# Performance work log

Hardware: AMD Instinct MI355X
Metric: run time of the kernel (lower is better)

The kernel has to match this reference:

```python
import jax, jax.numpy as jnp
import numpy as np

NEG = -1e30  # finite stand-in for -inf in the sparse-softmax mask


def setup_inputs() -> dict:
    key = jax.random.key(0)
    kh, kwl, kwn, kn = jax.random.split(key, 4)
    B, S, D, E = 8, 4096, 1024, 64
    return {
        "h": jax.random.normal(kh, (B, S, D), dtype=jnp.float32),
        "Wl": jax.random.normal(kwl, (E, D), dtype=jnp.float32) * 0.02,
        "bl": jnp.zeros((E,), dtype=jnp.float32),
        "Wn": jax.random.normal(kwn, (E, D), dtype=jnp.float32) * 0.02,
        "bn": jnp.zeros((E,), dtype=jnp.float32),
        "noise": jax.random.normal(kn, (B, S, E), dtype=jnp.float32),
        "top_k": 2,
    }


def reference(h, Wl, bl, Wn, bn, noise, top_k):
    # logits, noise std: two small linears over the expert dim
    logits = jnp.einsum("bsd,ed->bse", h, Wl) + bl          # [B,S,E]
    std = jax.nn.softplus(jnp.einsum("bsd,ed->bse", h, Wn) + bn)
    noisy = logits + noise * std                              # [B,S,E]

    full_p = jax.nn.softmax(noisy, axis=-1)

    topk_vals, ix = jax.lax.top_k(noisy, top_k)               # [B,S,k]
    E = noisy.shape[-1]
    # scatter top-k values back into a -inf-filled tensor == mask non-topk
    mask = jax.nn.one_hot(ix, E, dtype=jnp.bool_).any(axis=-2)  # [B,S,E]
    sparse = jnp.where(mask, noisy, NEG)
    route_p = jax.nn.softmax(sparse, axis=-1)
    return route_p, ix, full_p
```

## Files before the change

### kernel.cpp

```cpp
#include <hip/hip_runtime.h>
#include <math.h>


#define DIM 1024
#define NEXP 64
#define CS 132
#define LOSCALE 2048.0f
#define INV_LOSCALE (1.0f / 2048.0f)

using half8v   = __attribute__((ext_vector_type(8)))  _Float16;
using floatx16 = __attribute__((ext_vector_type(16))) float;

#define MFMA32(a, b, c) __builtin_amdgcn_mfma_f32_32x32x16_f16((a), (b), (c), 0, 0, 0)

__global__ __launch_bounds__(512)
void prep_B(const float* __restrict__ Wl, const float* __restrict__ Wn,
            _Float16* __restrict__ Bp)
{
    const int idx = blockIdx.x * 512 + threadIdx.x;
    const int r  = idx >> 7;
    const int c2 = idx & 127;
    const float* W = (r < 64) ? (Wl + (size_t)r * DIM) : (Wn + (size_t)(r - 64) * DIM);
    float f[8];
    *(float4*)(f)     = *(const float4*)(W + c2 * 8);
    *(float4*)(f + 4) = *(const float4*)(W + c2 * 8 + 4);
    half8v hi, lo;
#pragma unroll
    for (int i = 0; i < 8; i++) {
        _Float16 hh = (_Float16)f[i];
        hi[i] = hh;
        lo[i] = (_Float16)((f[i] - (float)hh) * LOSCALE);
    }
    const int t = c2 >> 1, hf = c2 & 1;
    _Float16* base = Bp + ((size_t)t * 128 + r) * 32 + hf * 16;
    *(half8v*)(base)     = hi;
    *(half8v*)(base + 8) = lo;
}

__global__ __launch_bounds__(256, 4)
void router_fused(const float* __restrict__ h, const _Float16* __restrict__ Bp,
                  const float* __restrict__ bl, const float* __restrict__ bn,
                  const float* __restrict__ noise,
                  float* __restrict__ outR, float* __restrict__ outIx,
                  float* __restrict__ outF)
{
    __shared__ float Cs[32 * CS];

    const int tid   = threadIdx.x;
    const int wv    = tid >> 6;
    const int lane  = tid & 63;
    const int row31 = lane & 31;
    const int oct   = lane >> 5;
    const int colb  = wv * 32;
    const int tok0  = blockIdx.x * 32;

    const float*    aP = h  + (size_t)(tok0 + row31) * DIM + oct * 8;
    const _Float16* bP = Bp + (size_t)(colb + row31) * 32 + oct * 16;

    floatx16 acc1, acc2;
#pragma unroll
    for (int i = 0; i < 16; i++) { acc1[i] = 0.f; acc2[i] = 0.f; }

#define LOADA(s, A0, A1) do {                                                  \
        (A0) = *(const float4*)(aP + (s) * 16);                                \
        (A1) = *(const float4*)(aP + (s) * 16 + 4);                            \
    } while (0)
#define LOADB(s, BH, BL) do {                                                  \
        (BH) = *(const half8v*)(bP + (size_t)(s) * 4096);                      \
        (BL) = *(const half8v*)(bP + (size_t)(s) * 4096 + 8);                  \
    } while (0)
#define STEP(A0, A1, BH, BL) do {                                              \
        float f_[8] = {(A0).x, (A0).y, (A0).z, (A0).w,                         \
                       (A1).x, (A1).y, (A1).z, (A1).w};                        \
        half8v aH_, aL_;                                                       \
        _Pragma("unroll")                                                      \
        for (int i_ = 0; i_ < 8; i_++) {                                       \
            _Float16 hh_ = (_Float16)f_[i_];                                   \
            aH_[i_] = hh_;                                                     \
            aL_[i_] = (_Float16)((f_[i_] - (float)hh_) * LOSCALE);             \
        }                                                                      \
        acc1 = MFMA32(aH_, (BH), acc1);                                        \
        acc2 = MFMA32(aH_, (BL), acc2);                                        \
        acc2 = MFMA32(aL_, (BH), acc2);                                        \
    } while (0)

    float4 aE0, aE1, aO0, aO1;
    half8v bHE, bLE, bHO, bLO;
    LOADA(0, aE0, aE1); LOADB(0, bHE, bLE);
    LOADA(1, aO0, aO1); LOADB(1, bHO, bLO);

    for (int tb = 0; tb < 31; ++tb) {
        const int s = 2 * tb;
        STEP(aE0, aE1, bHE, bLE);
        LOADA(s + 2, aE0, aE1); LOADB(s + 2, bHE, bLE);
        STEP(aO0, aO1, bHO, bLO);
        LOADA(s + 3, aO0, aO1); LOADB(s + 3, bHO, bLO);
    }
    STEP(aE0, aE1, bHE, bLE);
    STEP(aO0, aO1, bHO, bLO);

#undef STEP
#undef LOADB
#undef LOADA

#pragma unroll
    for (int i = 0; i < 16; i++) {
        const int rowt = (i & 3) + 8 * (i >> 2) + 4 * oct;
        Cs[rowt * CS + colb + row31] = acc1[i] + acc2[i] * INV_LOSCALE;
    }
    __syncthreads();

    const float blv = bl[lane];
    const float bnv = bn[lane];

    for (int t = wv; t < 32; t += 4) {
        const int gt = tok0 + t;
        float xr = Cs[t * CS + lane] + blv;
        float xf = Cs[t * CS + 64 + lane] + bnv;
        float nz = noise[(size_t)gt * NEXP + lane];

        float stdv = fmaxf(xf, 0.f) + log1pf(expf(-fabsf(xf)));
        float noisy = fmaf(nz, stdv, xr);

        float v = noisy; int idx = lane;
#pragma unroll
        for (int o = 32; o > 0; o >>= 1) {
            float ov = __shfl_xor(v, o, 64);
            int   oi = __shfl_xor(idx, o, 64);
            if (ov > v || (ov == v && oi < idx)) { v = ov; idx = oi; }
        }
        const float v1 = v; const int i1 = idx;

        float p = expf(noisy - v1);
        float s = p;
#pragma unroll
        for (int o = 32; o > 0; o >>= 1) s += __shfl_xor(s, o, 64);
        float fullp = p / s;

        v = (lane == i1) ? -INFINITY : noisy; idx = lane;
#pragma unroll
        for (int o = 32; o > 0; o >>= 1) {
            float ov = __shfl_xor(v, o, 64);
            int   oi = __shfl_xor(idx, o, 64);
            if (ov > v || (ov == v && oi < idx)) { v = ov; idx = oi; }
        }
        const float v2 = v; const int i2 = idx;

        float e2 = expf(v2 - v1);
        float den = 1.f + e2;
        float routep = (lane == i1) ? (1.f / den) : ((lane == i2) ? (e2 / den) : 0.f);

        outR[(size_t)gt * NEXP + lane] = routep;
        outF[(size_t)gt * NEXP + lane] = fullp;
        if (lane == 0) {
            outIx[(size_t)gt * 2 + 0] = (float)i1;
            outIx[(size_t)gt * 2 + 1] = (float)i2;
        }
    }
}

extern "C" void kernel_launch(void* const* d_in, const int* in_sizes, int n_in,
                              void* d_out, int out_size, void* d_ws, size_t ws_size,
                              hipStream_t stream) {
    const float* h     = (const float*)d_in[0];
    const float* Wl    = (const float*)d_in[1];
    const float* bl    = (const float*)d_in[2];
    const float* Wn    = (const float*)d_in[3];
    const float* bn    = (const float*)d_in[4];
    const float* noise = (const float*)d_in[5];
    float* out = (float*)d_out;

    const int M = in_sizes[0] / DIM;
    float* outR  = out;
    float* outIx = out + (size_t)M * NEXP;
    float* outF  = outIx + (size_t)M * 2;

    _Float16* Bp = (_Float16*)d_ws;

    prep_B<<<32, 512, 0, stream>>>(Wl, Wn, Bp);
    router_fused<<<M / 32, 256, 0, stream>>>(h, Bp, bl, bn, noise, outR, outIx, outF);
}
```

Measured before the change: 293.3 us.

## Stage A tile hi/lo split once into double-buffered LDS shared across waves

Previously every wave loaded the same 32 token rows of h from global memory and redid the fp32-to-fp16 hi/lo split, giving 4x redundant loads and conversions per block. Now the block loads A cooperatively, splits it once, writes it to double-buffered LDS, and each wave reads its MFMA operands from LDS while the next tile is loaded and converted. This adds a barrier per 64-wide K tile and LDS traffic. The LDS is reused as the output staging buffer afterwards.

```diff
diff --git a/kernel.cpp b/kernel.cpp
--- a/kernel.cpp
+++ b/kernel.cpp
@@ -7,11 +7,17 @@
 #define CS 132
 #define LOSCALE 2048.0f
 #define INV_LOSCALE (1.0f / 2048.0f)
+#define AROW 272
+#define ABUF 8704
 
 using half8v   = __attribute__((ext_vector_type(8)))  _Float16;
 using floatx16 = __attribute__((ext_vector_type(16))) float;
 
 #define MFMA32(a, b, c) __builtin_amdgcn_mfma_f32_32x32x16_f16((a), (b), (c), 0, 0, 0)
+
+#define WAITLGKM0 asm volatile("s_waitcnt lgkmcnt(0)" ::: "memory")
+#define SCHED0    __builtin_amdgcn_sched_barrier(0)
+#define BAR       __builtin_amdgcn_s_barrier()
 
 __global__ __launch_bounds__(512)
 void prep_B(const float* __restrict__ Wl, const float* __restrict__ Wn,
@@ -44,7 +50,7 @@
                   float* __restrict__ outR, float* __restrict__ outIx,
                   float* __restrict__ outF)
 {
-    __shared__ float Cs[32 * CS];
+    __shared__ __align__(16) char lds_raw[2 * ABUF];
 
     const int tid   = threadIdx.x;
     const int wv    = tid >> 6;
@@ -54,55 +60,107 @@
     const int colb  = wv * 32;
     const int tok0  = blockIdx.x * 32;
 
-    const float*    aP = h  + (size_t)(tok0 + row31) * DIM + oct * 8;
+    const int rSt = tid >> 3, f8 = tid & 7;
+    const float* aStage = h + (size_t)(tok0 + rSt) * DIM + f8 * 8;
+    const int aWhi = rSt * AROW + f8 * 16;
+
     const _Float16* bP = Bp + (size_t)(colb + row31) * 32 + oct * 16;
 
+    const int rdHi = row31 * AROW;
+
     floatx16 acc1, acc2;
 #pragma unroll
     for (int i = 0; i < 16; i++) { acc1[i] = 0.f; acc2[i] = 0.f; }
 
-#define LOADA(s, A0, A1) do {                                                  \
-        (A0) = *(const float4*)(aP + (s) * 16);                                \
-        (A1) = *(const float4*)(aP + (s) * 16 + 4);                            \
-    } while (0)
-#define LOADB(s, BH, BL) do {                                                  \
-        (BH) = *(const half8v*)(bP + (size_t)(s) * 4096);                      \
-        (BL) = *(const half8v*)(bP + (size_t)(s) * 4096 + 8);                  \
-    } while (0)
-#define STEP(A0, A1, BH, BL) do {                                              \
+#define LOADA(t, A0, A1) do {                                                  \
+        (A0) = *(const float4*)(aStage + (t) * 64);                            \
+        (A1) = *(const float4*)(aStage + (t) * 64 + 4);                        \
+    } while (0)
+
+#define SPLITW(bufc, A0, A1) do {                                              \
         float f_[8] = {(A0).x, (A0).y, (A0).z, (A0).w,                         \
                        (A1).x, (A1).y, (A1).z, (A1).w};                        \
-        half8v aH_, aL_;                                                       \
+        half8v hi_, lo_;                                                       \
         _Pragma("unroll")                                                      \
         for (int i_ = 0; i_ < 8; i_++) {                                       \
             _Float16 hh_ = (_Float16)f_[i_];                                   \
-            aH_[i_] = hh_;                                                     \
-            aL_[i_] = (_Float16)((f_[i_] - (float)hh_) * LOSCALE);             \
+            hi_[i_] = hh_;                                                     \
+            lo_[i_] = (_Float16)((f_[i_] - (float)hh_) * LOSCALE);             \
         }                                                                      \
+        *(half8v*)((bufc) + aWhi)       = hi_;                                 \
+        *(half8v*)((bufc) + aWhi + 128) = lo_;                                 \
+    } while (0)
+
+#define ISSUE_B(t) do {                                                        \
+        const _Float16* bs_ = bP + (size_t)(t) * 16384;                        \
+        bh0 = *(const half8v*)(bs_);                                           \
+        bl0 = *(const half8v*)(bs_ + 8);                                       \
+        bh1 = *(const half8v*)(bs_ + 4096);                                    \
+        bl1 = *(const half8v*)(bs_ + 4104);                                    \
+        bh2 = *(const half8v*)(bs_ + 8192);                                    \
+        bl2 = *(const half8v*)(bs_ + 8200);                                    \
+        bh3 = *(const half8v*)(bs_ + 12288);                                   \
+        bl3 = *(const half8v*)(bs_ + 12296);                                   \
+    } while (0)
+
+#define SUBSTEP(bufc, ss, BH, BL) do {                                         \
+        const int co_ = ((ss) * 2 + oct) << 4;                                 \
+        const half8v aH_ = *(const half8v*)((bufc) + rdHi + co_);              \
+        const half8v aL_ = *(const half8v*)((bufc) + rdHi + co_ + 128);        \
         acc1 = MFMA32(aH_, (BH), acc1);                                        \
         acc2 = MFMA32(aH_, (BL), acc2);                                        \
         acc2 = MFMA32(aL_, (BH), acc2);                                        \
     } while (0)
 
+#define COMPUTE(bufc) do {                                                     \
+        SUBSTEP(bufc, 0, bh0, bl0);                                            \
+        SUBSTEP(bufc, 1, bh1, bl1);                                            \
+        SUBSTEP(bufc, 2, bh2, bl2);                                            \
+        SUBSTEP(bufc, 3, bh3, bl3);                                            \
+    } while (0)
+
+    half8v bh0, bl0, bh1, bl1, bh2, bl2, bh3, bl3;
+    char* const buf0 = lds_raw;
+    char* const buf1 = lds_raw + ABUF;
     float4 aE0, aE1, aO0, aO1;
-    half8v bHE, bLE, bHO, bLO;
-    LOADA(0, aE0, aE1); LOADB(0, bHE, bLE);
-    LOADA(1, aO0, aO1); LOADB(1, bHO, bLO);
-
-    for (int tb = 0; tb < 31; ++tb) {
-        const int s = 2 * tb;
-        STEP(aE0, aE1, bHE, bLE);
-        LOADA(s + 2, aE0, aE1); LOADB(s + 2, bHE, bLE);
-        STEP(aO0, aO1, bHO, bLO);
-        LOADA(s + 3, aO0, aO1); LOADB(s + 3, bHO, bLO);
-    }
-    STEP(aE0, aE1, bHE, bLE);
-    STEP(aO0, aO1, bHO, bLO);
-
-#undef STEP
-#undef LOADB
+
+    LOADA(0, aE0, aE1);
+    SPLITW(buf0, aE0, aE1);
+    LOADA(1, aO0, aO1);
+    WAITLGKM0; SCHED0;
+    BAR; SCHED0;
+
+#define BODY_W_L(t, CBUF, NBUF, AW0, AW1, AL0, AL1) do {                       \
+        ISSUE_B(t);                                                            \
+        SPLITW(NBUF, AW0, AW1);                                                \
+        LOADA((t) + 2, AL0, AL1);                                              \
+        COMPUTE(CBUF);                                                         \
+        WAITLGKM0; SCHED0;                                                     \
+        BAR; SCHED0;                                                           \
+    } while (0)
+
+    for (int tb = 0; tb < 7; ++tb) {
+        const int t0 = 2 * tb;
+        BODY_W_L(t0,     buf0, buf1, aO0, aO1, aE0, aE1);
+        BODY_W_L(t0 + 1, buf1, buf0, aE0, aE1, aO0, aO1);
+    }
+    ISSUE_B(14);
+    SPLITW(buf1, aO0, aO1);
+    COMPUTE(buf0);
+    WAITLGKM0; SCHED0;
+    BAR; SCHED0;
+    ISSUE_B(15);
+    COMPUTE(buf1);
+    __syncthreads();
+
+#undef BODY_W_L
+#undef COMPUTE
+#undef SUBSTEP
+#undef ISSUE_B
+#undef SPLITW
 #undef LOADA
 
+    float* Cs = (float*)lds_raw;
 #pragma unroll
     for (int i = 0; i < 16; i++) {
         const int rowt = (i & 3) + 8 * (i >> 2) + 4 * oct;
```

Measured after the change: 252.6 us. -13.9%, faster.
